# Optimization experiments

Hardware: AMD Instinct MI355X
Metric: run time of the kernel (lower is better)

The kernel has to match this reference:

```python
import jax, jax.numpy as jnp
import numpy as np

B, T, D = 8, 2048, 64

def setup_inputs() -> dict:
    key = jax.random.key(0)
    kq, kv, kk = jax.random.split(key, 3)
    q = jax.random.normal(kq, (B, T, D), dtype=jnp.float32)
    v = jax.random.normal(kv, (B, T, D), dtype=jnp.float32)
    k = jax.random.normal(kk, (B, T, D), dtype=jnp.float32)
    q_mask = jnp.ones((B, T), dtype=bool)
    v_mask = jnp.ones((B, T), dtype=bool)
    return {"q": q, "v": v, "k": k, "q_mask": q_mask, "v_mask": v_mask}


def reference(q, v, k, q_mask, v_mask):
    # scores: [B, Tq, Tk] -- dot-product attention scores (q @ k^T)
    scores = jnp.einsum('bqd,bkd->bqk', q, k)
    Tq, Tk = scores.shape[-2], scores.shape[-1]
    # causal lower-triangular mask merged (logical AND) with value mask
    causal_mask = jnp.tril(jnp.ones((Tq, Tk), dtype=bool))          # [Tq, Tk]
    scores_mask = causal_mask[None, :, :] & v_mask[:, None, :]       # [B, Tq, Tk]
    # masking via large-constant subtraction, as in the original
    scores = scores - 1e9 * (~scores_mask).astype(scores.dtype)
    weights = jax.nn.softmax(scores, axis=-1)                        # [B, Tq, Tk]
    # dropout=0.0 / inference path: weights used as-is
    result = jnp.einsum('bqk,bkd->bqd', weights, v)                  # [B, Tq, D]
    result = result * q_mask[:, :, None].astype(result.dtype)
    return weights, result
```

## Files before the change

kernel.cpp:

```cpp
#include <hip/hip_runtime.h>
#include <hip/hip_bf16.h>


#define TT 2048
#define DD 64
#define PP 72
#define KV_U16 12288
#define V_OFF_U16 8192
#define LOG2E 1.4426950408889634f

typedef unsigned short u16;
typedef unsigned int u32;
typedef __attribute__((ext_vector_type(8))) short short8;
typedef __attribute__((ext_vector_type(4))) float f32x4;

#define MFMA16(a, b, c) __builtin_amdgcn_mfma_f32_16x16x32_bf16((a), (b), (c), 0, 0, 0)

#if __has_builtin(__builtin_amdgcn_exp2f)
#define EXP2F(x) __builtin_amdgcn_exp2f(x)
#else
#define EXP2F(x) exp2f(x)
#endif

static __device__ __forceinline__ u32 pkbf(float a, float b) {
    __hip_bfloat162 h = __float22bfloat162_rn(make_float2(a, b));
    u32 u; __builtin_memcpy(&u, &h, 4); return u;
}
static __device__ __forceinline__ float fbits(u32 i) {
    union { u32 i; float f; } c; c.i = i; return c.f;
}

static __device__ __forceinline__ void qhalf(const float* __restrict__ qp,
                                             short8& ho, short8& lo_) {
    float4 x0 = *(const float4*)qp;
    float4 x1 = *(const float4*)(qp + 4);
    float f[8] = {x0.x, x0.y, x0.z, x0.w, x1.x, x1.y, x1.z, x1.w};
    u32 h[4], l[4];
    #pragma unroll
    for (int i = 0; i < 4; ++i) {
        const float e0 = f[2*i] * LOG2E, e1 = f[2*i+1] * LOG2E;
        h[i] = pkbf(e0, e1);
        l[i] = pkbf(e0 - fbits(h[i] << 16), e1 - fbits(h[i] & 0xffff0000u));
    }
    uint4 uh = make_uint4(h[0], h[1], h[2], h[3]);
    uint4 ul = make_uint4(l[0], l[1], l[2], l[3]);
    ho = *(short8*)&uh; lo_ = *(short8*)&ul;
}
static __device__ __forceinline__ void load_qfrag(const float* __restrict__ qrow, int koff,
        short8& h0o, short8& h1o, short8& l0o, short8& l1o) {
    qhalf(qrow + koff, h0o, l0o);
    qhalf(qrow + 32 + koff, h1o, l1o);
}

__global__ __launch_bounds__(256) void prep_kernel(const float* __restrict__ v,
                                                   const float* __restrict__ k,
                                                   u16* __restrict__ ws) {
    const int bt = (int)blockIdx.x;
    const int b = bt >> 5, t = bt & 31;
    const int tid = (int)threadIdx.x;
    u16* wt = ws + (size_t)bt * KV_U16;
    {
        const int r = tid >> 2, c0 = (tid & 3) * 16;
        const float* g = k + ((size_t)b * TT + t * 64 + r) * DD + c0;
        float f[16];
        #pragma unroll
        for (int i = 0; i < 4; ++i) {
            float4 u = *(const float4*)(g + 4 * i);
            f[4*i] = u.x; f[4*i+1] = u.y; f[4*i+2] = u.z; f[4*i+3] = u.w;
        }
        u32 hi[8], lo[8];
        #pragma unroll
        for (int i = 0; i < 8; ++i) {
            hi[i] = pkbf(f[2*i], f[2*i+1]);
            lo[i] = pkbf(f[2*i] - fbits(hi[i] << 16), f[2*i+1] - fbits(hi[i] & 0xffff0000u));
        }
        const int rgrp = r >> 4, lo4 = r & 15;
        const int p = c0 >> 5;
        const int q0 = (c0 & 31) >> 3;
        uint4* w4 = (uint4*)wt;
        const int ih = ((rgrp * 4 + p) * 4 + q0) * 16 + lo4;
        w4[ih]      = make_uint4(hi[0], hi[1], hi[2], hi[3]);
        w4[ih + 16] = make_uint4(hi[4], hi[5], hi[6], hi[7]);
        const int il = ((rgrp * 4 + p + 2) * 4 + q0) * 16 + lo4;
        w4[il]      = make_uint4(lo[0], lo[1], lo[2], lo[3]);
        w4[il + 16] = make_uint4(lo[4], lo[5], lo[6], lo[7]);
    }
    {
        const int d = tid & 63, g4 = tid >> 6;
        const float* gv = v + ((size_t)b * TT + t * 64 + g4 * 16) * DD + d;
        u32 pk[8];
        #pragma unroll
        for (int m = 0; m < 8; ++m)
            pk[m] = pkbf(gv[(size_t)(2 * m) * DD], gv[(size_t)(2 * m + 1) * DD]);
        const int dgrp = d >> 4, lo4d = d & 15;
        const int kc = g4 >> 1, q0 = (g4 & 1) * 2;
        uint4* w4 = (uint4*)(wt + V_OFF_U16);
        const int iv = ((dgrp * 2 + kc) * 4 + q0) * 16 + lo4d;
        w4[iv]      = make_uint4(pk[0], pk[1], pk[2], pk[3]);
        w4[iv + 16] = make_uint4(pk[4], pk[5], pk[6], pk[7]);
    }
}

__global__ __launch_bounds__(512, 4) void attn_kernel(
    const float* __restrict__ q, const u16* __restrict__ ws,
    float* __restrict__ wout, float* __restrict__ rout)
{
    __shared__ __align__(16) u16 lds_p[2][2][32 * PP];
    __shared__ float lds_rowsum[8][32];
    __shared__ float lds_l2s[32];
    float* const lds_o = (float*)&lds_p[0][0][0];

    const int tid  = (int)threadIdx.x;
    const int w    = tid >> 6;
    const int sub  = w >> 2;
    const int wl   = w & 3;
    const int lane = tid & 63;
    const int quad = lane >> 4;
    const int lo4  = lane & 15;
    const int w16  = wl * 16;
    const int koff = quad * 8;

    const int b = (int)blockIdx.x & 7;
    const int p = (int)blockIdx.x >> 3;
    const int ta = p, tb = 127 - p;
    const int kta_last = ta >> 2;
    const int ktb_last = tb >> 2;
    const int q0a = ta * 16, q0b = tb * 16;

    const float* qb = q + (size_t)b * TT * DD;
    const u16* wsb = ws + (size_t)b * 32 * KV_U16;
    const size_t bq = (size_t)b * TT;

    short8 ahA0, ahA1, alA0, alA1, ahB0, ahB1, alB0, alB1;
    load_qfrag(qb + (size_t)(q0a + lo4) * DD, koff, ahA0, ahA1, alA0, alA1);
    load_qfrag(qb + (size_t)(q0b + lo4) * DD, koff, ahB0, ahB1, alB0, alB1);

    float sumA = 0.f, sumB = 0.f;
    {
        const u16* kfp = wsb + (size_t)sub * KV_U16 + wl * 2048 + lane * 8;
        #pragma unroll 2
        for (int kt = sub; kt <= ktb_last; kt += 2, kfp += 2 * KV_U16) {
            const short8 bh0 = *(const short8*)(kfp);
            const short8 bh1 = *(const short8*)(kfp + 512);
            const short8 bl0 = *(const short8*)(kfp + 1024);
            const short8 bl1 = *(const short8*)(kfp + 1536);
            const int kbase = kt * 64 + w16 + quad * 4;
            if (kt <= kta_last) {
                f32x4 cs = {0.f, 0.f, 0.f, 0.f};
                cs = MFMA16(bh0, ahA0, cs); cs = MFMA16(bh1, ahA1, cs);
                cs = MFMA16(bh0, alA0, cs); cs = MFMA16(bh1, alA1, cs);
                cs = MFMA16(bl0, ahA0, cs); cs = MFMA16(bl1, ahA1, cs);
                if (kt * 64 + 63 <= q0a) {
                    sumA += EXP2F(cs[0]) + EXP2F(cs[1]) + EXP2F(cs[2]) + EXP2F(cs[3]);
                } else {
                    #pragma unroll
                    for (int reg = 0; reg < 4; ++reg)
                        if (kbase + reg <= q0a + lo4) sumA += EXP2F(cs[reg]);
                }
            }
            {
                f32x4 cs = {0.f, 0.f, 0.f, 0.f};
                cs = MFMA16(bh0, ahB0, cs); cs = MFMA16(bh1, ahB1, cs);
                cs = MFMA16(bh0, alB0, cs); cs = MFMA16(bh1, alB1, cs);
                cs = MFMA16(bl0, ahB0, cs); cs = MFMA16(bl1, ahB1, cs);
                if (kt * 64 + 63 <= q0b) {
                    sumB += EXP2F(cs[0]) + EXP2F(cs[1]) + EXP2F(cs[2]) + EXP2F(cs[3]);
                } else {
                    #pragma unroll
                    for (int reg = 0; reg < 4; ++reg)
                        if (kbase + reg <= q0b + lo4) sumB += EXP2F(cs[reg]);
                }
            }
        }
    }
    sumA += __shfl_xor(sumA, 16, 64); sumA += __shfl_xor(sumA, 32, 64);
    sumB += __shfl_xor(sumB, 16, 64); sumB += __shfl_xor(sumB, 32, 64);
    if (lane < 16) {
        lds_rowsum[w][lane]      = sumA;
        lds_rowsum[w][16 + lane] = sumB;
    }
    __syncthreads();
    if (tid < 32) {
        float s = 0.f;
        #pragma unroll
        for (int i = 0; i < 8; ++i) s += lds_rowsum[i][tid];
        lds_l2s[tid] = __log2f(s);
    }
    __syncthreads();
    const float l2sA = lds_l2s[lo4], l2sB = lds_l2s[16 + lo4];

    f32x4 coA = {0.f, 0.f, 0.f, 0.f}, coB = {0.f, 0.f, 0.f, 0.f};
    {
        float* const wrowA = wout + (bq + q0a + lo4) * TT;
        float* const wrowB = wout + (bq + q0b + lo4) * TT;
        const u16* kfp = wsb + (size_t)sub * KV_U16 + wl * 2048 + lane * 8;
        const u16* vfp = wsb + (size_t)sub * KV_U16 + V_OFF_U16 + wl * 1024 + lane * 8;
        short8 kh0 = *(const short8*)(kfp);
        short8 kh1 = *(const short8*)(kfp + 512);
        short8 kl0 = *(const short8*)(kfp + 1024);
        short8 kl1 = *(const short8*)(kfp + 1536);
        int par = 0;
        for (int kt0 = 0; kt0 <= ktb_last; kt0 += 2) {
            const int kt = kt0 + sub;
            const bool actB = (kt <= ktb_last);
            const bool actA = (kt <= kta_last);
            const bool nact = (kt + 2 <= ktb_last);
            short8 va0, va1, nh0, nh1, nl0, nl1;
            if (actB) {
                va0 = *(const short8*)(vfp);
                va1 = *(const short8*)(vfp + 512);
            }
            if (nact) {
                nh0 = *(const short8*)(kfp + 2 * KV_U16);
                nh1 = *(const short8*)(kfp + 2 * KV_U16 + 512);
                nl0 = *(const short8*)(kfp + 2 * KV_U16 + 1024);
                nl1 = *(const short8*)(kfp + 2 * KV_U16 + 1536);
            }
            if (actB) {
                const int kbase = kt * 64 + w16 + quad * 4;
                if (actA) {
                    f32x4 cs = {0.f, 0.f, 0.f, 0.f};
                    cs = MFMA16(kh0, ahA0, cs); cs = MFMA16(kh1, ahA1, cs);
                    cs = MFMA16(kh0, alA0, cs); cs = MFMA16(kh1, alA1, cs);
                    cs = MFMA16(kl0, ahA0, cs); cs = MFMA16(kl1, ahA1, cs);
                    float e0, e1, e2, e3;
                    if (kt * 64 + 63 <= q0a) {
                        e0 = EXP2F(cs[0] - l2sA); e1 = EXP2F(cs[1] - l2sA);
                        e2 = EXP2F(cs[2] - l2sA); e3 = EXP2F(cs[3] - l2sA);
                    } else {
                        e0 = (kbase + 0 <= q0a + lo4) ? EXP2F(cs[0] - l2sA) : 0.f;
                        e1 = (kbase + 1 <= q0a + lo4) ? EXP2F(cs[1] - l2sA) : 0.f;
                        e2 = (kbase + 2 <= q0a + lo4) ? EXP2F(cs[2] - l2sA) : 0.f;
                        e3 = (kbase + 3 <= q0a + lo4) ? EXP2F(cs[3] - l2sA) : 0.f;
                    }
                    *(float4*)&wrowA[kbase] = make_float4(e0, e1, e2, e3);
                    *(uint2*)&lds_p[sub][par][lo4 * PP + w16 + quad * 4] =
                        make_uint2(pkbf(e0, e1), pkbf(e2, e3));
                }
                {
                    f32x4 cs = {0.f, 0.f, 0.f, 0.f};
                    cs = MFMA16(kh0, ahB0, cs); cs = MFMA16(kh1, ahB1, cs);
                    cs = MFMA16(kh0, alB0, cs); cs = MFMA16(kh1, alB1, cs);
                    cs = MFMA16(kl0, ahB0, cs); cs = MFMA16(kl1, ahB1, cs);
                    float e0, e1, e2, e3;
                    if (kt * 64 + 63 <= q0b) {
                        e0 = EXP2F(cs[0] - l2sB); e1 = EXP2F(cs[1] - l2sB);
                        e2 = EXP2F(cs[2] - l2sB); e3 = EXP2F(cs[3] - l2sB);
                    } else {
                        e0 = (kbase + 0 <= q0b + lo4) ? EXP2F(cs[0] - l2sB) : 0.f;
                        e1 = (kbase + 1 <= q0b + lo4) ? EXP2F(cs[1] - l2sB) : 0.f;
                        e2 = (kbase + 2 <= q0b + lo4) ? EXP2F(cs[2] - l2sB) : 0.f;
                        e3 = (kbase + 3 <= q0b + lo4) ? EXP2F(cs[3] - l2sB) : 0.f;
                    }
                    *(float4*)&wrowB[kbase] = make_float4(e0, e1, e2, e3);
                    *(uint2*)&lds_p[sub][par][(16 + lo4) * PP + w16 + quad * 4] =
                        make_uint2(pkbf(e0, e1), pkbf(e2, e3));
                }
            }
            asm volatile("s_waitcnt lgkmcnt(0)" ::: "memory");
            __builtin_amdgcn_s_barrier();
            __builtin_amdgcn_sched_barrier(0);
            if (actB) {
                const u16* pb = &lds_p[sub][par][0];
                if (actA) {
                    const short8 bv0 = *(const short8*)&pb[lo4 * PP + koff];
                    const short8 bv1 = *(const short8*)&pb[lo4 * PP + 32 + koff];
                    coA = MFMA16(va0, bv0, coA);
                    coA = MFMA16(va1, bv1, coA);
                }
                {
                    const short8 bv0 = *(const short8*)&pb[(16 + lo4) * PP + koff];
                    const short8 bv1 = *(const short8*)&pb[(16 + lo4) * PP + 32 + koff];
                    coB = MFMA16(va0, bv0, coB);
                    coB = MFMA16(va1, bv1, coB);
                }
            }
            par ^= 1;
            if (nact) {
                kh0 = nh0; kh1 = nh1; kl0 = nl0; kl1 = nl1;
                kfp += 2 * KV_U16; vfp += 2 * KV_U16;
            }
        }
    }

    __syncthreads();
    if (sub == 1) {
        *(float4*)&lds_o[(lo4) * 68 + w16 + quad * 4]      = make_float4(coA[0], coA[1], coA[2], coA[3]);
        *(float4*)&lds_o[(16 + lo4) * 68 + w16 + quad * 4] = make_float4(coB[0], coB[1], coB[2], coB[3]);
    }
    __syncthreads();
    if (sub == 0) {
        const float4 oa = *(const float4*)&lds_o[(lo4) * 68 + w16 + quad * 4];
        const float4 ob = *(const float4*)&lds_o[(16 + lo4) * 68 + w16 + quad * 4];
        float4 ra = make_float4(coA[0] + oa.x, coA[1] + oa.y, coA[2] + oa.z, coA[3] + oa.w);
        float4 rb = make_float4(coB[0] + ob.x, coB[1] + ob.y, coB[2] + ob.z, coB[3] + ob.w);
        *(float4*)&rout[(bq + q0a + lo4) * DD + w16 + quad * 4] = ra;
        *(float4*)&rout[(bq + q0b + lo4) * DD + w16 + quad * 4] = rb;
    }

    {
        const int zr = tid >> 5, zc = tid & 31;
        const float4 z = make_float4(0.f, 0.f, 0.f, 0.f);
        float4* ra = (float4*)(wout + (bq + q0a + zr) * TT);
        for (int c4 = (((kta_last + 1) * 64) >> 2) + zc; c4 < TT / 4; c4 += 32) ra[c4] = z;
        float4* rb = (float4*)(wout + (bq + q0b + zr) * TT);
        for (int c4 = (((ktb_last + 1) * 64) >> 2) + zc; c4 < TT / 4; c4 += 32) rb[c4] = z;
    }
}

extern "C" void kernel_launch(void* const* d_in, const int* in_sizes, int n_in,
                              void* d_out, int out_size, void* d_ws, size_t ws_size,
                              hipStream_t stream) {
    const float* q = (const float*)d_in[0];
    const float* v = (const float*)d_in[1];
    const float* k = (const float*)d_in[2];
    float* wout = (float*)d_out;
    float* rout = wout + (size_t)8 * TT * TT;
    u16* ws = (u16*)d_ws;
    prep_kernel<<<dim3(256), dim3(256), 0, stream>>>(v, k, ws);
    attn_kernel<<<dim3(512), dim3(512), 0, stream>>>(q, ws, wout, rout);
}
```

Before: 172.7 us.

## Write attention weights coalesced from LDS tile and prefetch V fragments

The fp32 weights output is no longer stored straight from the MFMA accumulator layout, where each lane wrote four floats into a different row. After the barrier, the bf16 probability tile already staged in LDS is read back in a row-contiguous layout, widened to fp32 and stored, so 16 lanes cover one contiguous row segment. V fragments are also double-buffered in registers alongside the K prefetch, so they load one iteration ahead. The weights output now carries bf16 rounding instead of full fp32 values, which lowers its precision. The extra LDS reads add some pressure inside the loop.

After: 170.1 us. No clear change (-1.5%).

```diff
diff --git a/kernel.cpp b/kernel.cpp
--- a/kernel.cpp
+++ b/kernel.cpp
@@ -29,6 +29,7 @@
 static __device__ __forceinline__ float fbits(u32 i) {
     union { u32 i; float f; } c; c.i = i; return c.f;
 }
+static __device__ __forceinline__ float bf2f(u16 u) { return fbits(((u32)u) << 16); }
 
 static __device__ __forceinline__ void qhalf(const float* __restrict__ qp,
                                              short8& ho, short8& lo_) {
@@ -191,30 +192,30 @@
 
     f32x4 coA = {0.f, 0.f, 0.f, 0.f}, coB = {0.f, 0.f, 0.f, 0.f};
     {
-        float* const wrowA = wout + (bq + q0a + lo4) * TT;
-        float* const wrowB = wout + (bq + q0b + lo4) * TT;
+        const int wr = lane >> 4, c4 = lane & 15;
+        const int sr = wl * 4 + wr;
         const u16* kfp = wsb + (size_t)sub * KV_U16 + wl * 2048 + lane * 8;
         const u16* vfp = wsb + (size_t)sub * KV_U16 + V_OFF_U16 + wl * 1024 + lane * 8;
         short8 kh0 = *(const short8*)(kfp);
         short8 kh1 = *(const short8*)(kfp + 512);
         short8 kl0 = *(const short8*)(kfp + 1024);
         short8 kl1 = *(const short8*)(kfp + 1536);
+        short8 va0 = *(const short8*)(vfp);
+        short8 va1 = *(const short8*)(vfp + 512);
         int par = 0;
         for (int kt0 = 0; kt0 <= ktb_last; kt0 += 2) {
             const int kt = kt0 + sub;
             const bool actB = (kt <= ktb_last);
             const bool actA = (kt <= kta_last);
             const bool nact = (kt + 2 <= ktb_last);
-            short8 va0, va1, nh0, nh1, nl0, nl1;
-            if (actB) {
-                va0 = *(const short8*)(vfp);
-                va1 = *(const short8*)(vfp + 512);
-            }
+            short8 nh0, nh1, nl0, nl1, nv0, nv1;
             if (nact) {
                 nh0 = *(const short8*)(kfp + 2 * KV_U16);
                 nh1 = *(const short8*)(kfp + 2 * KV_U16 + 512);
                 nl0 = *(const short8*)(kfp + 2 * KV_U16 + 1024);
                 nl1 = *(const short8*)(kfp + 2 * KV_U16 + 1536);
+                nv0 = *(const short8*)(vfp + 2 * KV_U16);
+                nv1 = *(const short8*)(vfp + 2 * KV_U16 + 512);
             }
             if (actB) {
                 const int kbase = kt * 64 + w16 + quad * 4;
@@ -233,7 +234,6 @@
                         e2 = (kbase + 2 <= q0a + lo4) ? EXP2F(cs[2] - l2sA) : 0.f;
                         e3 = (kbase + 3 <= q0a + lo4) ? EXP2F(cs[3] - l2sA) : 0.f;
                     }
-                    *(float4*)&wrowA[kbase] = make_float4(e0, e1, e2, e3);
                     *(uint2*)&lds_p[sub][par][lo4 * PP + w16 + quad * 4] =
                         make_uint2(pkbf(e0, e1), pkbf(e2, e3));
                 }
@@ -252,7 +252,6 @@
                         e2 = (kbase + 2 <= q0b + lo4) ? EXP2F(cs[2] - l2sB) : 0.f;
                         e3 = (kbase + 3 <= q0b + lo4) ? EXP2F(cs[3] - l2sB) : 0.f;
                     }
-                    *(float4*)&wrowB[kbase] = make_float4(e0, e1, e2, e3);
                     *(uint2*)&lds_p[sub][par][(16 + lo4) * PP + w16 + quad * 4] =
                         make_uint2(pkbf(e0, e1), pkbf(e2, e3));
                 }
@@ -261,16 +260,31 @@
             __builtin_amdgcn_s_barrier();
             __builtin_amdgcn_sched_barrier(0);
             if (actB) {
-                const u16* pb = &lds_p[sub][par][0];
+                const u16* pbuf = &lds_p[sub][par][0];
+                const int colb = kt * 64 + c4 * 4;
                 if (actA) {
-                    const short8 bv0 = *(const short8*)&pb[lo4 * PP + koff];
-                    const short8 bv1 = *(const short8*)&pb[lo4 * PP + 32 + koff];
+                    const uint2 pr = *(const uint2*)&pbuf[sr * PP + c4 * 4];
+                    float4 o;
+                    o.x = bf2f((u16)pr.x); o.y = bf2f((u16)(pr.x >> 16));
+                    o.z = bf2f((u16)pr.y); o.w = bf2f((u16)(pr.y >> 16));
+                    *(float4*)&wout[(bq + q0a + sr) * TT + colb] = o;
+                }
+                {
+                    const uint2 pr = *(const uint2*)&pbuf[(16 + sr) * PP + c4 * 4];
+                    float4 o;
+                    o.x = bf2f((u16)pr.x); o.y = bf2f((u16)(pr.x >> 16));
+                    o.z = bf2f((u16)pr.y); o.w = bf2f((u16)(pr.y >> 16));
+                    *(float4*)&wout[(bq + q0b + sr) * TT + colb] = o;
+                }
+                if (actA) {
+                    const short8 bv0 = *(const short8*)&pbuf[lo4 * PP + koff];
+                    const short8 bv1 = *(const short8*)&pbuf[lo4 * PP + 32 + koff];
                     coA = MFMA16(va0, bv0, coA);
                     coA = MFMA16(va1, bv1, coA);
                 }
                 {
-                    const short8 bv0 = *(const short8*)&pb[(16 + lo4) * PP + koff];
-                    const short8 bv1 = *(const short8*)&pb[(16 + lo4) * PP + 32 + koff];
+                    const short8 bv0 = *(const short8*)&pbuf[(16 + lo4) * PP + koff];
+                    const short8 bv1 = *(const short8*)&pbuf[(16 + lo4) * PP + 32 + koff];
                     coB = MFMA16(va0, bv0, coB);
                     coB = MFMA16(va1, bv1, coB);
                 }
@@ -278,6 +292,7 @@
             par ^= 1;
             if (nact) {
                 kh0 = nh0; kh1 = nh1; kl0 = nl0; kl1 = nl1;
+                va0 = nv0; va1 = nv1;
                 kfp += 2 * KV_U16; vfp += 2 * KV_U16;
             }
         }
```
